# Performance work log

Hardware: AMD Instinct MI355X
Metric: run time of the kernel (lower is better)

## Reference

```python
import jax, jax.numpy as jnp
import numpy as np

B, N, C, G, K = 4, 6000, 91, 32, 100
IMG = 800.0
SCORE_TH = 0.05
NMS_TH = 0.5
MATCH_TH = 0.5
MIN_SIZE = 0.01
BBOX_CLIP = float(np.log(1000.0 / 16.0))
WX, WY, WW, WH = 10.0, 10.0, 5.0, 5.0


def _make_boxes(key, shape_prefix):
    k1, k2 = jax.random.split(key)
    xy = jax.random.uniform(k1, shape_prefix + (2,), minval=0.0, maxval=IMG - 130.0)
    wh = jax.random.uniform(k2, shape_prefix + (2,), minval=8.0, maxval=128.0)
    return jnp.concatenate([xy, xy + wh], axis=-1)


def setup_inputs() -> dict:
    key = jax.random.key(0)
    k1, k2, k3, k4, k5 = jax.random.split(key, 5)
    return {
        "class_logits": 2.0 * jax.random.normal(k1, (B * N, C), dtype=jnp.float32),
        "box_regression": jax.random.normal(k2, (B * N, C * 4), dtype=jnp.float32),
        "proposals": _make_boxes(k3, (B, N)),
        "gt_boxes": _make_boxes(k4, (B, G)),
        "gt_labels": jax.random.randint(k5, (B, G), 1, C),
    }


def _box_iou(a, b):
    # a [G,4], b [N,4] -> [G,N]
    area_a = (a[:, 2] - a[:, 0]) * (a[:, 3] - a[:, 1])
    area_b = (b[:, 2] - b[:, 0]) * (b[:, 3] - b[:, 1])
    lt = jnp.maximum(a[:, None, :2], b[None, :, :2])
    rb = jnp.minimum(a[:, None, 2:], b[None, :, 2:])
    wh = jnp.clip(rb - lt, 0.0)
    inter = wh[..., 0] * wh[..., 1]
    return inter / (area_a[:, None] + area_b[None, :] - inter)


def _decode(rel, props):
    # torchvision BoxCoder.decode; rel [N,C,4], props [N,4]
    w = props[:, 2] - props[:, 0]
    h = props[:, 3] - props[:, 1]
    cx = props[:, 0] + 0.5 * w
    cy = props[:, 1] + 0.5 * h
    dx = rel[..., 0] / WX
    dy = rel[..., 1] / WY
    dw = jnp.minimum(rel[..., 2] / WW, BBOX_CLIP)
    dh = jnp.minimum(rel[..., 3] / WH, BBOX_CLIP)
    pcx = dx * w[:, None] + cx[:, None]
    pcy = dy * h[:, None] + cy[:, None]
    pw = jnp.exp(dw) * w[:, None]
    ph = jnp.exp(dh) * h[:, None]
    return jnp.stack([pcx - 0.5 * pw, pcy - 0.5 * ph, pcx + 0.5 * pw, pcy + 0.5 * ph], axis=-1)


def _image(logits, reg, props, gtb, gtl):
    # --- assign_targets_to_proposals (Matcher, low=high=0.5, no low-quality matches) ---
    iou = _box_iou(gtb, props)                      # [G, N]
    best = iou.max(axis=0)
    mi = jnp.argmax(iou, axis=0)
    matched = jnp.where(best >= MATCH_TH, mi, -1)   # -1 == BELOW_LOW_THRESHOLD
    assigned = jnp.where(matched >= 0, gtl[jnp.clip(matched, 0)], 0)

    # --- postprocess_detections ---
    scores = jax.nn.softmax(logits, axis=-1)[:, 1:].reshape(-1)                       # [N*(C-1)]
    boxes = jnp.clip(_decode(reg.reshape(N, C, 4), props)[:, 1:], 0.0, IMG)
    boxes = boxes.reshape(-1, 4)                                                      # [N*(C-1),4]
    labels = jnp.tile(jnp.arange(1, C), N)                                            # [N*(C-1)]
    ws = boxes[:, 2] - boxes[:, 0]
    hs = boxes[:, 3] - boxes[:, 1]
    valid = (scores > SCORE_TH) & (ws >= MIN_SIZE) & (hs >= MIN_SIZE)
    s0 = jnp.where(valid, scores, -jnp.inf)
    # batched_nms trick: offset boxes by label so cross-class IoU is 0
    off = boxes + (labels.astype(boxes.dtype) * (IMG + 1.0))[:, None]
    off_area = (off[:, 2] - off[:, 0]) * (off[:, 3] - off[:, 1])

    def step(s, _):
        i = jnp.argmax(s)
        sc = s[i]
        b = off[i]
        lt = jnp.maximum(off[:, :2], b[:2])
        rb = jnp.minimum(off[:, 2:], b[2:])
        wh = jnp.clip(rb - lt, 0.0)
        inter = wh[:, 0] * wh[:, 1]
        iou_all = inter / (off_area + (b[2] - b[0]) * (b[3] - b[1]) - inter)
        s = jnp.where(iou_all > NMS_TH, -jnp.inf, s)  # suppress (includes self)
        ok = jnp.isfinite(sc)
        ob = jnp.where(ok, boxes[i], 0.0)
        osc = jnp.where(ok, sc, 0.0)
        ol = jnp.where(ok, labels[i], -1)
        return s, (ob, osc, ol)

    _, (kb, ksc, kl) = jax.lax.scan(step, s0, None, length=K)
    return kb, ksc, kl, assigned, matched


def reference(class_logits, box_regression, proposals, gt_boxes, gt_labels):
    logits = class_logits.reshape(B, N, C)
    reg = box_regression.reshape(B, N, C * 4)
    kb, ksc, kl, assigned, matched = jax.vmap(_image)(logits, reg, proposals, gt_boxes, gt_labels)
    dets = jnp.concatenate([kb, ksc[..., None]], axis=-1)  # [B, K, 5]
    return dets, kl, assigned, matched
```

## Files before the change

### kernel.cpp

```cpp
#include <hip/hip_runtime.h>
#include <math.h>

#define NB 4
#define NN 6000
#define NC 91
#define NG 32
#define NK 100
#define NCLS (NC - 1)
#define NBUC (NB * NCLS)
#define SLOTS_MAX 2048
#define CUR_STRIDE 32
#define PMAX 512
#define MATW 256
#define MPB 4096
#define RS_BLOCKS 6000

#define SCORE_TH 0.05f
#define NMS_TH 0.5f
#define MATCH_TH 0.5f
#define MIN_SIZE 0.01f
#define BBOX_CLIP 4.135166556742356f
#define C_SUP 0.5000000298023223876953125

#define CFENCE() asm volatile("" ::: "memory")

__device__ __forceinline__ bool decode_one(
    const float* __restrict__ reg, const float* __restrict__ props,
    float l, float m, float s0, int row, int c, float out[5])
{
    float score = __fdiv_rn(expf(__fsub_rn(l, m)), s0);

    const float4 p = *reinterpret_cast<const float4*>(props + (size_t)row * 4);
    float w  = __fsub_rn(p.z, p.x);
    float h  = __fsub_rn(p.w, p.y);
    float cx = __fadd_rn(p.x, __fmul_rn(0.5f, w));
    float cy = __fadd_rn(p.y, __fmul_rn(0.5f, h));

    const float4 r4 = *reinterpret_cast<const float4*>(
        reg + (size_t)row * (NC * 4) + (size_t)c * 4);
    float dx = __fdiv_rn(r4.x, 10.0f);
    float dy = __fdiv_rn(r4.y, 10.0f);
    float dw = fminf(__fdiv_rn(r4.z, 5.0f), BBOX_CLIP);
    float dh = fminf(__fdiv_rn(r4.w, 5.0f), BBOX_CLIP);

    float pcx = __fadd_rn(__fmul_rn(dx, w), cx);
    float pcy = __fadd_rn(__fmul_rn(dy, h), cy);
    float pw  = __fmul_rn(expf(dw), w);
    float ph  = __fmul_rn(expf(dh), h);

    float x1 = __fsub_rn(pcx, __fmul_rn(0.5f, pw));
    float y1 = __fsub_rn(pcy, __fmul_rn(0.5f, ph));
    float x2 = __fadd_rn(pcx, __fmul_rn(0.5f, pw));
    float y2 = __fadd_rn(pcy, __fmul_rn(0.5f, ph));
    x1 = fminf(fmaxf(x1, 0.0f), 800.0f);
    y1 = fminf(fmaxf(y1, 0.0f), 800.0f);
    x2 = fminf(fmaxf(x2, 0.0f), 800.0f);
    y2 = fminf(fmaxf(y2, 0.0f), 800.0f);

    out[0] = score; out[1] = x1; out[2] = y1; out[3] = x2; out[4] = y2;
    float ws_ = __fsub_rn(x2, x1);
    float hs_ = __fsub_rn(y2, y1);
    return (score > SCORE_TH) && (ws_ >= MIN_SIZE) && (hs_ >= MIN_SIZE);
}

__global__ __launch_bounds__(256) void fused_kernel(
    const float* __restrict__ logits, const float* __restrict__ reg,
    const float* __restrict__ props, const float* __restrict__ gtb,
    const int* __restrict__ gtl,
    float* __restrict__ out_assigned, float* __restrict__ out_matched,
    int* __restrict__ cursors, float* __restrict__ ent, int slots)
{
    int bid = blockIdx.x;
    if (bid < RS_BLOCKS) {
        int wid = threadIdx.x >> 6, lane = threadIdx.x & 63;
        int row = bid * 4 + wid;
        const float* rp = logits + (size_t)row * NC;
        float l0 = rp[lane];
        float l1 = (lane < NC - 64) ? rp[64 + lane] : -INFINITY;
        float m = fmaxf(fmaxf(-INFINITY, l0), l1);
        for (int o = 32; o; o >>= 1) m = fmaxf(m, __shfl_down(m, o));
        m = __shfl(m, 0);
        float s = __fadd_rn(__fadd_rn(0.0f, expf(__fsub_rn(l0, m))),
                            expf(__fsub_rn(l1, m)));
        for (int o = 32; o; o >>= 1) s = __fadd_rn(s, __shfl_down(s, o));
        float s0 = __shfl(s, 0);
        float thr = __fadd_rn(m, logf(__fmul_rn(0.04f, s0)));

        int b = row / NN;
        int nprop = row - b * NN;

        if (lane >= 1 && l0 > thr) {
            float o[5];
            if (decode_one(reg, props, l0, m, s0, row, lane, o)) {
                int c = lane;
                int g = b * NCLS + (c - 1);
                int pos = atomicAdd(&cursors[g * CUR_STRIDE], 1);
                if (pos < slots) {
                    float* e = ent + ((size_t)g * slots + pos) * 8;
                    *reinterpret_cast<float4*>(e) =
                        make_float4(o[1], o[2], o[3], o[4]);
                    *reinterpret_cast<float2*>(e + 4) =
                        make_float2(o[0], (float)(nprop * NCLS + (c - 1)));
                }
            }
        }
        if (lane < NC - 64 && l1 > thr) {
            float o[5];
            int c = lane + 64;
            if (decode_one(reg, props, l1, m, s0, row, c, o)) {
                int g = b * NCLS + (c - 1);
                int pos = atomicAdd(&cursors[g * CUR_STRIDE], 1);
                if (pos < slots) {
                    float* e = ent + ((size_t)g * slots + pos) * 8;
                    *reinterpret_cast<float4*>(e) =
                        make_float4(o[1], o[2], o[3], o[4]);
                    *reinterpret_cast<float2*>(e + 4) =
                        make_float2(o[0], (float)(nprop * NCLS + (c - 1)));
                }
            }
        }
    } else {
        int t = (bid - RS_BLOCKS) * 256 + threadIdx.x;
        if (t >= NB * NN) return;
        int b = t / NN;
        const float4 p = *reinterpret_cast<const float4*>(props + (size_t)t * 4);
        float parea = __fmul_rn(__fsub_rn(p.z, p.x), __fsub_rn(p.w, p.y));
        float best = -1.0f; int bi = -1;
        for (int g = 0; g < NG; ++g) {
            const float4 q = *reinterpret_cast<const float4*>(gtb + ((size_t)b * NG + g) * 4);
            float garea = __fmul_rn(__fsub_rn(q.z, q.x), __fsub_rn(q.w, q.y));
            float ltx = fmaxf(q.x, p.x), lty = fmaxf(q.y, p.y);
            float rbx = fminf(q.z, p.z), rby = fminf(q.w, p.w);
            float wx = fmaxf(__fsub_rn(rbx, ltx), 0.0f);
            float wy = fmaxf(__fsub_rn(rby, lty), 0.0f);
            float inter = __fmul_rn(wx, wy);
            float iou = __fdiv_rn(inter, __fsub_rn(__fadd_rn(garea, parea), inter));
            if (iou > best) { best = iou; bi = g; }
        }
        int matched = (best >= MATCH_TH) ? bi : -1;
        int assigned = (matched >= 0) ? gtl[b * NG + matched] : 0;
        out_matched[t]  = (float)matched;
        out_assigned[t] = (float)assigned;
    }
}

__device__ void nms_glb(int g, int n, float* __restrict__ E, float tb, float cls,
                        float* __restrict__ selbuf, int* __restrict__ selcnt)
{
    int lane = threadIdx.x & 63;
    int kout = 0;
    for (int k = 0; k < NK; ++k) {
        float bv = -INFINITY, boi = INFINITY; int bi = -1;
        for (int i = lane; i < n; i += 64) {
            float v = E[(size_t)i * 8 + 4], oi = E[(size_t)i * 8 + 5];
            if (v > bv || (v == bv && oi < boi)) { bv = v; boi = oi; bi = i; }
        }
        int wl = lane;
        for (int o = 1; o < 64; o <<= 1) {
            float v2 = __shfl_xor(bv, o); float o2 = __shfl_xor(boi, o);
            int l2 = __shfl_xor(wl, o);
            bool bt = (v2 > bv) || (v2 == bv && o2 < boi);
            bv = bt ? v2 : bv; boi = bt ? o2 : boi; wl = bt ? l2 : wl;
        }
        if (bv == -INFINITY) break;
        int wi = __shfl(bi, wl);
        float sx1 = E[(size_t)wi * 8 + 0], sy1 = E[(size_t)wi * 8 + 1];
        float sx2 = E[(size_t)wi * 8 + 2], sy2 = E[(size_t)wi * 8 + 3];
        if (lane == wl) {
            float* so = selbuf + ((size_t)g * NK + k) * 8;
            so[0] = bv; so[1] = sx1; so[2] = sy1; so[3] = sx2; so[4] = sy2;
            so[5] = cls; so[6] = boi; so[7] = 0.0f;
        }
        float bx1 = __fadd_rn(sx1, tb), by1 = __fadd_rn(sy1, tb);
        float bx2 = __fadd_rn(sx2, tb), by2 = __fadd_rn(sy2, tb);
        float sar = __fmul_rn(__fsub_rn(bx2, bx1), __fsub_rn(by2, by1));
        for (int i = lane; i < n; i += 64) {
            float v = E[(size_t)i * 8 + 4];
            if (v == -INFINITY) continue;
            float ox1 = __fadd_rn(E[(size_t)i * 8 + 0], tb);
            float oy1 = __fadd_rn(E[(size_t)i * 8 + 1], tb);
            float ox2 = __fadd_rn(E[(size_t)i * 8 + 2], tb);
            float oy2 = __fadd_rn(E[(size_t)i * 8 + 3], tb);
            float oar = __fmul_rn(__fsub_rn(ox2, ox1), __fsub_rn(oy2, oy1));
            float ltx = fmaxf(ox1, bx1), lty = fmaxf(oy1, by1);
            float rbx = fminf(ox2, bx2), rby = fminf(oy2, by2);
            float wx = fmaxf(__fsub_rn(rbx, ltx), 0.0f);
            float wy = fmaxf(__fsub_rn(rby, lty), 0.0f);
            float inter = __fmul_rn(wx, wy);
            float den = __fsub_rn(__fadd_rn(oar, sar), inter);
            if ((double)inter > C_SUP * (double)den) E[(size_t)i * 8 + 4] = -INFINITY;
        }
        kout = k + 1;
    }
    if (lane == 0) selcnt[g] = kout;
}

template <int CAP>
__device__ __forceinline__ float selN(const float a[CAP], int j) {
    float r = a[0];
#pragma unroll
    for (int i = 1; i < CAP; ++i) r = (j == i) ? a[i] : r;
    return r;
}
__device__ __forceinline__ float rdlane(float v, int l) {
    return __uint_as_float(
        (unsigned)__builtin_amdgcn_readlane((int)__float_as_uint(v), l));
}

template <int CAP>
__device__ __forceinline__ int sweep_reg(
    int lane, int n, float tb,
    const float* sx1, const float* sy1, const float* sx2, const float* sy2,
    int* acc)
{
    float ox1[CAP], oy1[CAP], ox2[CAP], oy2[CAP], oar[CAP];
    unsigned alive = 0;
#pragma unroll
    for (int j = 0; j < CAP; ++j) {
        int sidx = lane * CAP + j;
        if (sidx < n) {
            float a  = __fadd_rn(sx1[sidx], tb);
            float b_ = __fadd_rn(sy1[sidx], tb);
            float c_ = __fadd_rn(sx2[sidx], tb);
            float d_ = __fadd_rn(sy2[sidx], tb);
            ox1[j] = a; oy1[j] = b_; ox2[j] = c_; oy2[j] = d_;
            oar[j] = __fmul_rn(__fsub_rn(c_, a), __fsub_rn(d_, b_));
            alive |= 1u << j;
        } else {
            ox1[j] = 0.f; oy1[j] = 0.f; ox2[j] = 0.f; oy2[j] = 0.f; oar[j] = 0.f;
        }
    }
    int kout = 0;
    while (kout < NK) {
        unsigned long long bal = __ballot(alive != 0u);
        if (!bal) break;
        int fl = (int)__ffsll(bal) - 1;
        unsigned am = (unsigned)__builtin_amdgcn_readlane((int)alive, fl);
        int js = __ffs(am) - 1;
        float bx1 = rdlane(selN<CAP>(ox1, js), fl);
        float by1 = rdlane(selN<CAP>(oy1, js), fl);
        float bx2 = rdlane(selN<CAP>(ox2, js), fl);
        float by2 = rdlane(selN<CAP>(oy2, js), fl);
        float bar = rdlane(selN<CAP>(oar, js), fl);
        if (lane == 0) acc[kout] = fl * CAP + js;
        kout++;
        unsigned kill = 0;
#pragma unroll
        for (int j = 0; j < CAP; ++j) {
            float ltx = fmaxf(ox1[j], bx1), lty = fmaxf(oy1[j], by1);
            float rbx = fminf(ox2[j], bx2), rby = fminf(oy2[j], by2);
            float wx = fmaxf(__fsub_rn(rbx, ltx), 0.0f);
            float wy = fmaxf(__fsub_rn(rby, lty), 0.0f);
            float inter = __fmul_rn(wx, wy);
            float den = __fsub_rn(__fadd_rn(oar[j], bar), inter);
            if ((double)inter > C_SUP * (double)den) kill |= 1u << j;
        }
        alive &= ~kill;
    }
    return kout;
}

__global__ __launch_bounds__(256) void bucket_nms_kernel(
    const int* __restrict__ cursors, int slots,
    float* __restrict__ entries,
    float* __restrict__ selbuf, int* __restrict__ selcnt)
{
    int g = blockIdx.x;
    int n = cursors[g * CUR_STRIDE]; if (n > slots) n = slots;
    int tid = threadIdx.x;
    if (n == 0) { if (tid == 0) selcnt[g] = 0; return; }
    float* E = entries + (size_t)g * slots * 8;
    float cls = (float)(g % NCLS + 1);
    float tb = __fmul_rn(cls, 801.0f);

    if (n > PMAX) {
        if (tid < 64) nms_glb(g, n, E, tb, cls, selbuf, selcnt);
        return;
    }

    __shared__ unsigned skhi[PMAX], sklo[PMAX];
    __shared__ int sperm[PMAX];
    __shared__ float sx1[PMAX], sy1[PMAX], sx2[PMAX], sy2[PMAX];
    __shared__ unsigned long long dmask[MATW * 4];
    __shared__ int acc[NK];
    __shared__ int s_kout, s_fb;

    int P = 64; while (P < n) P <<= 1;

    for (int i = tid; i < P; i += 256) {
        if (i < n) {
            const float2 kv = *reinterpret_cast<const float2*>(E + (size_t)i * 8 + 4);
            skhi[i] = __float_as_uint(kv.x);
            sklo[i] = ~((unsigned)kv.y);
        } else { skhi[i] = 0u; sklo[i] = 0u; }
        sperm[i] = i;
    }
    __syncthreads();
    for (int k = 2; k <= P; k <<= 1) {
        for (int j = k >> 1; j > 0; j >>= 1) {
            bool cross = (j >= 128);
            if (cross) __syncthreads();
            for (int t = tid; t < (P >> 1); t += 256) {
                int i = ((t & ~(j - 1)) << 1) | (t & (j - 1));
                int l = i | j;
                unsigned ah = skhi[i], al = sklo[i], ch = skhi[l], cl_ = sklo[l];
                bool alt = (ah < ch) || (ah == ch && al < cl_);
                bool agt = (ah > ch) || (ah == ch && al > cl_);
                bool sw = ((i & k) == 0) ? alt : agt;
                if (sw) {
                    skhi[i] = ch; sklo[i] = cl_; skhi[l] = ah; sklo[l] = al;
                    int tp = sperm[i]; sperm[i] = sperm[l]; sperm[l] = tp;
                }
            }
            if (cross) __syncthreads();
            else CFENCE();
        }
    }
    __syncthreads();
    for (int i = tid; i < n; i += 256) {
        const float4 v = *reinterpret_cast<const float4*>(E + (size_t)sperm[i] * 8);
        sx1[i] = v.x; sy1[i] = v.y; sx2[i] = v.z; sy2[i] = v.w;
    }
    __syncthreads();

    int W = (n < MATW) ? n : MATW;
    int nchunk = (W + 63) >> 6;
    int wv = tid >> 6, lane = tid & 63;

    float jx1[4], jy1[4], jx2[4], jy2[4], jar[4];
#pragma unroll
    for (int c = 0; c < 4; ++c) {
        int j = c * 64 + lane;
        if (j < W) {
            float a  = __fadd_rn(sx1[j], tb);
            float b_ = __fadd_rn(sy1[j], tb);
            float c_ = __fadd_rn(sx2[j], tb);
            float d_ = __fadd_rn(sy2[j], tb);
            jx1[c] = a; jy1[c] = b_; jx2[c] = c_; jy2[c] = d_;
            jar[c] = __fmul_rn(__fsub_rn(c_, a), __fsub_rn(d_, b_));
        } else {
            jx1[c] = 0.f; jy1[c] = 0.f; jx2[c] = 0.f; jy2[c] = 0.f; jar[c] = 0.f;
        }
    }
    {
        int i0 = wv;
        float nx1 = 0.f, ny1 = 0.f, nx2 = 0.f, ny2 = 0.f;
        if (i0 < W) { nx1 = sx1[i0]; ny1 = sy1[i0]; nx2 = sx2[i0]; ny2 = sy2[i0]; }
        for (int i = i0; i < W; i += 4) {
            float rx1 = nx1, ry1 = ny1, rx2 = nx2, ry2 = ny2;
            int ni = i + 4;
            if (ni < W) { nx1 = sx1[ni]; ny1 = sy1[ni]; nx2 = sx2[ni]; ny2 = sy2[ni]; }
            float bx1 = __fadd_rn(rx1, tb), by1 = __fadd_rn(ry1, tb);
            float bx2 = __fadd_rn(rx2, tb), by2 = __fadd_rn(ry2, tb);
            float bar = __fmul_rn(__fsub_rn(bx2, bx1), __fsub_rn(by2, by1));
            int ic = i >> 6;
#pragma unroll
            for (int c = 0; c < 4; ++c) {
                if (c >= ic && c < nchunk) {
                    bool jv = (c * 64 + lane) < W;
                    float ltx = fmaxf(jx1[c], bx1), lty = fmaxf(jy1[c], by1);
                    float rbx = fminf(jx2[c], bx2), rby = fminf(jy2[c], by2);
                    float wx = fmaxf(__fsub_rn(rbx, ltx), 0.0f);
                    float wy = fmaxf(__fsub_rn(rby, lty), 0.0f);
                    float inter = __fmul_rn(wx, wy);
                    float den = __fsub_rn(__fadd_rn(jar[c], bar), inter);
                    bool sup = jv && ((double)inter > C_SUP * (double)den);
                    unsigned long long w64 = __ballot(sup);
                    if (lane == 0) dmask[i * 4 + c] = w64;
                }
            }
        }
    }
    __syncthreads();

    if (tid < 64) {
        unsigned long long alive = 0ull;
        if (lane < nchunk) {
            int rem = W - (lane << 6);
            alive = (rem >= 64) ? ~0ull : ((1ull << rem) - 1ull);
        }
        int kout = 0;
        while (kout < NK) {
            unsigned long long bal = __ballot(alive != 0ull);
            if (!bal) break;
            int fl = (int)__ffsll(bal) - 1;
            unsigned long long am = __shfl(alive, fl);
            int js = (int)__ffsll(am) - 1;
            int cand = (fl << 6) + js;
            if (lane == 0) acc[kout] = cand;
            kout++;
            if (lane < nchunk) alive &= ~dmask[cand * 4 + lane];
        }
        if (lane == 0) {
            s_kout = kout;
            s_fb = (kout < NK && n > W) ? 1 : 0;
        }
    }
    __syncthreads();

    if (s_fb) {
        if (tid < 64) {
            int kout = sweep_reg<8>(lane, n, tb, sx1, sy1, sx2, sy2, acc);
            if (lane == 0) s_kout = kout;
        }
        __syncthreads();
    }

    int kc = s_kout;
    if (tid == 0) selcnt[g] = kc;
    for (int k = tid; k < kc; k += 256) {
        int cand = acc[k];
        float* so = selbuf + ((size_t)g * NK + k) * 8;
        so[0] = __uint_as_float(skhi[cand]);
        so[1] = sx1[cand]; so[2] = sy1[cand];
        so[3] = sx2[cand]; so[4] = sy2[cand];
        so[5] = cls; so[6] = (float)(~sklo[cand]); so[7] = 0.0f;
    }
}

__global__ __launch_bounds__(512) void merge_kernel(
    const float* __restrict__ selbuf, const int* __restrict__ selcnt,
    float* __restrict__ out_dets, float* __restrict__ out_kl)
{
    int b = blockIdx.x, tid = threadIdx.x;
    __shared__ int scnt[NCLS], soff[NCLS + 1];
    __shared__ unsigned akhi[512], aklo[512];
    __shared__ unsigned bkhi[MPB], bklo[MPB], bpay[MPB];
    __shared__ int s_T, s_cntA;
    __shared__ unsigned s_LBhi, s_LBlo;

    if (tid < NCLS) scnt[tid] = selcnt[b * NCLS + tid];
    if (tid == 0) s_T = 0;
    __syncthreads();
    if (tid == 0) {
        int a = 0, ca = 0;
        for (int c = 0; c < NCLS; ++c) {
            soff[c] = a; a += scnt[c];
            ca += (scnt[c] < 4 ? scnt[c] : 4);
        }
        soff[NCLS] = a; s_cntA = ca;
    }
    __syncthreads();
    int tot = soff[NCLS];

    if (tot == 0) {
        for (int z = tid; z < NK * 5; z += 512) out_dets[(size_t)b * NK * 5 + z] = 0.0f;
        for (int z = tid; z < NK; z += 512)     out_kl[(size_t)b * NK + z] = -1.0f;
        return;
    }

    {
        unsigned kh = 0u, kl = 0u;
        if (tid < NCLS * 4) {
            int c = tid >> 2, i = tid & 3;
            if (i < scnt[c]) {
                const float* e = selbuf + ((size_t)(b * NCLS + c) * NK + i) * 8;
                kh = __float_as_uint(e[0]); kl = ~((unsigned)e[6]);
            }
        }
        akhi[tid] = kh; aklo[tid] = kl;
    }
    __syncthreads();
    for (int k = 2; k <= 512; k <<= 1) {
        for (int j = k >> 1; j > 0; j >>= 1) {
            bool cross = (j >= 128);
            if (cross) __syncthreads();
            if (tid < 256) {
                int t = tid;
                int i = ((t & ~(j - 1)) << 1) | (t & (j - 1));
                int l = i | j;
                unsigned ah = akhi[i], al = aklo[i], ch = akhi[l], cl_ = aklo[l];
                bool alt = (ah < ch) || (ah == ch && al < cl_);
                bool agt = (ah > ch) || (ah == ch && al > cl_);
                bool sw = ((i & k) == 0) ? alt : agt;
                if (sw) {
                    akhi[i] = ch; aklo[i] = cl_; akhi[l] = ah; aklo[l] = al;
                }
            }
            if (cross) __syncthreads();
            else CFENCE();
        }
    }
    __syncthreads();
    if (tid == 0) {
        if (s_cntA >= NK) { s_LBhi = akhi[NK - 1]; s_LBlo = aklo[NK - 1]; }
        else              { s_LBhi = 0u;           s_LBlo = 0u; }
    }
    __syncthreads();
    unsigned LBhi = s_LBhi, LBlo = s_LBlo;

    for (int flat = tid; flat < tot; flat += 512) {
        int lo = 0, hi = NCLS - 1;
        while (lo < hi) { int mid = (lo + hi + 1) >> 1;
                          if (soff[mid] <= flat) lo = mid; else hi = mid - 1; }
        int c = lo, i = flat - soff[c];
        const float* e = selbuf + ((size_t)(b * NCLS + c) * NK + i) * 8;
        unsigned kh = __float_as_uint(e[0]), kl = ~((unsigned)e[6]);
        bool ge = (kh > LBhi) || (kh == LBhi && kl >= LBlo);
        if (ge) {
            int pos = atomicAdd(&s_T, 1);
            if (pos < MPB) { bkhi[pos] = kh; bklo[pos] = kl;
                             bpay[pos] = (unsigned)((c << 7) | i); }
        }
    }
    __syncthreads();
    int T = s_T;

    if (T > MPB) {
        if (tid >= 64) return;
        int lane = tid;
        int g0 = b * NCLS + lane;
        int g1 = (lane < NCLS - 64) ? g0 + 64 : -1;
        int c0 = scnt[lane];
        int c1 = (g1 >= 0) ? scnt[lane + 64] : 0;
        int p0 = 0, p1 = 0;
        unsigned long long k0c = 0, k1c = 0;
        if (p0 < c0) { const float* h = selbuf + ((size_t)g0 * NK) * 8;
            k0c = ((unsigned long long)__float_as_uint(h[0]) << 32) | (unsigned long long)(~(unsigned)h[6]); }
        if (g1 >= 0 && p1 < c1) { const float* h = selbuf + ((size_t)g1 * NK) * 8;
            k1c = ((unsigned long long)__float_as_uint(h[0]) << 32) | (unsigned long long)(~(unsigned)h[6]); }
        for (int k = 0; k < NK; ++k) {
            bool t1 = (k1c > k0c);
            unsigned long long bk = t1 ? k1c : k0c;
            int bslot = t1 ? (lane + 64) : lane;
            for (int o = 1; o < 64; o <<= 1) {
                unsigned long long k2 = __shfl_xor(bk, o);
                int b2 = __shfl_xor(bslot, o);
                if (k2 > bk) { bk = k2; bslot = b2; }
            }
            if (bk == 0ull) {
                for (int z = k * 5 + lane; z < NK * 5; z += 64)
                    out_dets[(size_t)b * NK * 5 + z] = 0.0f;
                for (int z = k + lane; z < NK; z += 64)
                    out_kl[(size_t)b * NK + z] = -1.0f;
                return;
            }
            int owner = bslot & 63;
            if (lane == owner) {
                bool isA = (bslot < 64);
                int gg = isA ? g0 : g1;
                int pp = isA ? p0 : p1;
                const float* e = selbuf + ((size_t)gg * NK + pp) * 8;
                size_t o = ((size_t)b * NK + k) * 5;
                out_dets[o + 0] = e[1]; out_dets[o + 1] = e[2];
                out_dets[o + 2] = e[3]; out_dets[o + 3] = e[4];
                out_dets[o + 4] = e[0];
                out_kl[(size_t)b * NK + k] = e[5];
                if (isA) {
                    p0++; k0c = 0;
                    if (p0 < c0) { const float* h = selbuf + ((size_t)g0 * NK + p0) * 8;
                        k0c = ((unsigned long long)__float_as_uint(h[0]) << 32) | (unsigned long long)(~(unsigned)h[6]); }
                } else {
                    p1++; k1c = 0;
                    if (p1 < c1) { const float* h = selbuf + ((size_t)g1 * NK + p1) * 8;
                        k1c = ((unsigned long long)__float_as_uint(h[0]) << 32) | (unsigned long long)(~(unsigned)h[6]); }
                }
            }
        }
        return;
    }

    int P = 128; while (P < T) P <<= 1;
    for (int i = T + tid; i < P; i += 512) { bkhi[i] = 0u; bklo[i] = 0u; bpay[i] = 0u; }
    __syncthreads();
    for (int k = 2; k <= P; k <<= 1) {
        for (int j = k >> 1; j > 0; j >>= 1) {
            bool cross = (j >= 128);
            if (cross) __syncthreads();
            for (int t = tid; t < (P >> 1); t += 512) {
                int i = ((t & ~(j - 1)) << 1) | (t & (j - 1));
                int l = i | j;
                unsigned ah = bkhi[i], al = bklo[i], ch = bkhi[l], cl_ = bklo[l];
                bool alt = (ah < ch) || (ah == ch && al < cl_);
                bool agt = (ah > ch) || (ah == ch && al > cl_);
                bool sw = ((i & k) == 0) ? alt : agt;
                if (sw) {
                    bkhi[i] = ch; bklo[i] = cl_; bkhi[l] = ah; bklo[l] = al;
                    unsigned tp = bpay[i]; bpay[i] = bpay[l]; bpay[l] = tp;
                }
            }
            if (cross) __syncthreads();
            else CFENCE();
        }
    }
    __syncthreads();
    int kc = (T < NK) ? T : NK;
    for (int k = tid; k < NK; k += 512) {
        size_t o = ((size_t)b * NK + k) * 5;
        if (k < kc) {
            unsigned pay = bpay[k];
            int c = (int)(pay >> 7), p = (int)(pay & 127);
            const float* e = selbuf + ((size_t)(b * NCLS + c) * NK + p) * 8;
            out_dets[o + 0] = e[1]; out_dets[o + 1] = e[2];
            out_dets[o + 2] = e[3]; out_dets[o + 3] = e[4];
            out_dets[o + 4] = e[0];
            out_kl[(size_t)b * NK + k] = e[5];
        } else {
            out_dets[o + 0] = 0.0f; out_dets[o + 1] = 0.0f;
            out_dets[o + 2] = 0.0f; out_dets[o + 3] = 0.0f;
            out_dets[o + 4] = 0.0f;
            out_kl[(size_t)b * NK + k] = -1.0f;
        }
    }
}

extern "C" void kernel_launch(void* const* d_in, const int* in_sizes, int n_in,
                              void* d_out, int out_size, void* d_ws, size_t ws_size,
                              hipStream_t stream) {
    const float* logits = (const float*)d_in[0];
    const float* reg    = (const float*)d_in[1];
    const float* props  = (const float*)d_in[2];
    const float* gtb    = (const float*)d_in[3];
    const int*   gtl    = (const int*)d_in[4];

    float* out          = (float*)d_out;
    float* out_dets     = out;
    float* out_kl       = out + NB * NK * 5;
    float* out_assigned = out_kl + NB * NK;
    float* out_matched  = out_assigned + NB * NN;

    char* ws = (char*)d_ws;
    int*   cursors = (int*)(ws + 0);
    int*   selcnt  = (int*)(ws + 49152);
    float* selbuf  = (float*)(ws + 53248);
    size_t off_ent = 1205248;

    long avail = (long)ws_size - (long)off_ent;
    long per_slot = 32L * NBUC;
    long slotsl = (avail > 0) ? avail / per_slot : 0;
    int slots = (int)((slotsl > SLOTS_MAX) ? SLOTS_MAX : (slotsl < 0 ? 0 : slotsl));

    float* entries = (float*)(ws + off_ent);

    hipMemsetAsync(cursors, 0, NBUC * CUR_STRIDE * sizeof(int), stream);
    const int MATCH_BLOCKS = (NB * NN + 255) / 256;
    fused_kernel<<<RS_BLOCKS + MATCH_BLOCKS, 256, 0, stream>>>(
        logits, reg, props, gtb, gtl, out_assigned, out_matched,
        cursors, entries, slots);
    bucket_nms_kernel<<<NBUC, 256, 0, stream>>>(
        cursors, slots, entries, selbuf, selcnt);
    merge_kernel<<<NB, 512, 0, stream>>>(selbuf, selcnt, out_dets, out_kl);
}
```

Before: 122.9 us.

## Split bucket NMS into sort/matrix kernel and a separate 64-thread sweep kernel

The per-bucket NMS kernel is split in two. The first kernel sorts, builds the suppression bitmask matrix and writes the matrix and permutation to global memory. A new single-wave kernel then runs the greedy sweep and any fallback. PMAX is raised so that larger buckets stay off the slow global-memory path, and SLOTS_MAX is halved. The aim is to stop a 256-thread block from idling while one wave does the serial sweep, at the cost of an extra launch, global round-trips and a larger workspace footprint.

After: 132.0 us. 1.07x slower.

```diff
diff --git a/kernel.cpp b/kernel.cpp
--- a/kernel.cpp
+++ b/kernel.cpp
@@ -8,9 +8,9 @@
 #define NK 100
 #define NCLS (NC - 1)
 #define NBUC (NB * NCLS)
-#define SLOTS_MAX 2048
+#define SLOTS_MAX 1024
 #define CUR_STRIDE 32
-#define PMAX 512
+#define PMAX 1024
 #define MATW 256
 #define MPB 4096
 #define RS_BLOCKS 6000
@@ -260,30 +260,33 @@
     return kout;
 }
 
-__global__ __launch_bounds__(256) void bucket_nms_kernel(
+__global__ __launch_bounds__(256) void sort_matrix_kernel(
     const int* __restrict__ cursors, int slots,
     float* __restrict__ entries,
+    unsigned* __restrict__ permG, unsigned long long* __restrict__ dmaskG,
+    int2* __restrict__ binfo,
     float* __restrict__ selbuf, int* __restrict__ selcnt)
 {
     int g = blockIdx.x;
     int n = cursors[g * CUR_STRIDE]; if (n > slots) n = slots;
     int tid = threadIdx.x;
-    if (n == 0) { if (tid == 0) selcnt[g] = 0; return; }
+    if (n == 0) {
+        if (tid == 0) { selcnt[g] = 0; binfo[g] = make_int2(1, 0); }
+        return;
+    }
     float* E = entries + (size_t)g * slots * 8;
     float cls = (float)(g % NCLS + 1);
     float tb = __fmul_rn(cls, 801.0f);
 
     if (n > PMAX) {
         if (tid < 64) nms_glb(g, n, E, tb, cls, selbuf, selcnt);
+        if (tid == 0) binfo[g] = make_int2(1, n);
         return;
     }
 
     __shared__ unsigned skhi[PMAX], sklo[PMAX];
     __shared__ int sperm[PMAX];
     __shared__ float sx1[PMAX], sy1[PMAX], sx2[PMAX], sy2[PMAX];
-    __shared__ unsigned long long dmask[MATW * 4];
-    __shared__ int acc[NK];
-    __shared__ int s_kout, s_fb;
 
     int P = 64; while (P < n) P <<= 1;
 
@@ -366,55 +369,79 @@
                     float den = __fsub_rn(__fadd_rn(jar[c], bar), inter);
                     bool sup = jv && ((double)inter > C_SUP * (double)den);
                     unsigned long long w64 = __ballot(sup);
-                    if (lane == 0) dmask[i * 4 + c] = w64;
+                    if (lane == 0) dmaskG[(size_t)g * PMAX + i * 4 + c] = w64;
                 }
             }
         }
     }
-    __syncthreads();
-
-    if (tid < 64) {
-        unsigned long long alive = 0ull;
-        if (lane < nchunk) {
-            int rem = W - (lane << 6);
-            alive = (rem >= 64) ? ~0ull : ((1ull << rem) - 1ull);
-        }
-        int kout = 0;
-        while (kout < NK) {
-            unsigned long long bal = __ballot(alive != 0ull);
-            if (!bal) break;
-            int fl = (int)__ffsll(bal) - 1;
-            unsigned long long am = __shfl(alive, fl);
-            int js = (int)__ffsll(am) - 1;
-            int cand = (fl << 6) + js;
-            if (lane == 0) acc[kout] = cand;
-            kout++;
-            if (lane < nchunk) alive &= ~dmask[cand * 4 + lane];
-        }
-        if (lane == 0) {
-            s_kout = kout;
-            s_fb = (kout < NK && n > W) ? 1 : 0;
-        }
-    }
-    __syncthreads();
-
-    if (s_fb) {
-        if (tid < 64) {
-            int kout = sweep_reg<8>(lane, n, tb, sx1, sy1, sx2, sy2, acc);
-            if (lane == 0) s_kout = kout;
+    for (int i = tid; i < n; i += 256) permG[(size_t)g * PMAX + i] = (unsigned)sperm[i];
+    if (tid == 0) binfo[g] = make_int2(0, n);
+}
+
+__global__ __launch_bounds__(64) void sweep_kernel(
+    int slots, const float* __restrict__ entries,
+    const unsigned* __restrict__ permG,
+    const unsigned long long* __restrict__ dmaskG,
+    const int2* __restrict__ binfo,
+    float* __restrict__ selbuf, int* __restrict__ selcnt)
+{
+    int g = blockIdx.x;
+    int lane = threadIdx.x;
+    int2 bi = binfo[g];
+    if (bi.x) return;
+    int n = bi.y;
+    const float* E = entries + (size_t)g * slots * 8;
+    float cls = (float)(g % NCLS + 1);
+    float tb = __fmul_rn(cls, 801.0f);
+
+    int W = (n < MATW) ? n : MATW;
+    int nchunk = (W + 63) >> 6;
+
+    __shared__ unsigned long long dm[MATW * 4];
+    __shared__ int acc[NK];
+    __shared__ float fx1[PMAX], fy1[PMAX], fx2[PMAX], fy2[PMAX];
+
+    for (int t = lane; t < W * 4; t += 64) dm[t] = dmaskG[(size_t)g * PMAX + t];
+    __syncthreads();
+
+    unsigned long long alive = 0ull;
+    if (lane < nchunk) {
+        int rem = W - (lane << 6);
+        alive = (rem >= 64) ? ~0ull : ((1ull << rem) - 1ull);
+    }
+    int kout = 0;
+    while (kout < NK) {
+        unsigned long long bal = __ballot(alive != 0ull);
+        if (!bal) break;
+        int fl = (int)__ffsll(bal) - 1;
+        unsigned long long am = __shfl(alive, fl);
+        int js = (int)__ffsll(am) - 1;
+        int cand = (fl << 6) + js;
+        if (lane == 0) acc[kout] = cand;
+        kout++;
+        if (lane < nchunk) alive &= ~dm[cand * 4 + lane];
+    }
+
+    if (kout < NK && n > W) {
+        for (int i = lane; i < n; i += 64) {
+            unsigned sl = permG[(size_t)g * PMAX + i];
+            const float4 v = *reinterpret_cast<const float4*>(E + (size_t)sl * 8);
+            fx1[i] = v.x; fy1[i] = v.y; fx2[i] = v.z; fy2[i] = v.w;
         }
         __syncthreads();
-    }
-
-    int kc = s_kout;
-    if (tid == 0) selcnt[g] = kc;
-    for (int k = tid; k < kc; k += 256) {
+        kout = sweep_reg<16>(lane, n, tb, fx1, fy1, fx2, fy2, acc);
+    }
+    __syncthreads();
+    if (lane == 0) selcnt[g] = kout;
+
+    for (int k = lane; k < kout; k += 64) {
         int cand = acc[k];
+        unsigned sl = permG[(size_t)g * PMAX + cand];
+        const float* e = E + (size_t)sl * 8;
         float* so = selbuf + ((size_t)g * NK + k) * 8;
-        so[0] = __uint_as_float(skhi[cand]);
-        so[1] = sx1[cand]; so[2] = sy1[cand];
-        so[3] = sx2[cand]; so[4] = sy2[cand];
-        so[5] = cls; so[6] = (float)(~sklo[cand]); so[7] = 0.0f;
+        so[0] = e[4];
+        so[1] = e[0]; so[2] = e[1]; so[3] = e[2]; so[4] = e[3];
+        so[5] = cls; so[6] = e[5]; so[7] = 0.0f;
     }
 }
 
@@ -622,8 +649,12 @@
     char* ws = (char*)d_ws;
     int*   cursors = (int*)(ws + 0);
     int*   selcnt  = (int*)(ws + 49152);
-    float* selbuf  = (float*)(ws + 53248);
-    size_t off_ent = 1205248;
+    int2*  binfo   = (int2*)(ws + 51200);
+    float* selbuf  = (float*)(ws + 57344);
+    unsigned* permG = (unsigned*)(ws + 1212416);
+    unsigned long long* dmaskG =
+        (unsigned long long*)(ws + 2686976);
+    size_t off_ent = 5636096;
 
     long avail = (long)ws_size - (long)off_ent;
     long per_slot = 32L * NBUC;
@@ -637,7 +668,9 @@
     fused_kernel<<<RS_BLOCKS + MATCH_BLOCKS, 256, 0, stream>>>(
         logits, reg, props, gtb, gtl, out_assigned, out_matched,
         cursors, entries, slots);
-    bucket_nms_kernel<<<NBUC, 256, 0, stream>>>(
-        cursors, slots, entries, selbuf, selcnt);
+    sort_matrix_kernel<<<NBUC, 256, 0, stream>>>(
+        cursors, slots, entries, permG, dmaskG, binfo, selbuf, selcnt);
+    sweep_kernel<<<NBUC, 64, 0, stream>>>(
+        slots, entries, permG, dmaskG, binfo, selbuf, selcnt);
     merge_kernel<<<NB, 512, 0, stream>>>(selbuf, selcnt, out_dets, out_kl);
 }
```

## Replace bitonic sort with rank sort and drop global-memory NMS fallback

Applied to the files above, without the earlier changes.

Replaces the in-shared-memory bitonic sort of per-bucket candidates with a counting (rank) sort in which each thread computes the rank of up to four elements by scanning all keys. PMAX is raised to 1024 and SLOTS_MAX lowered to 1024, so every bucket takes the shared-memory path and the slow single-wavefront global NMS fallback is removed. The register sweep capacity is doubled to cover the larger buckets. The trade-off is O(n^2) comparisons per bucket, more shared memory per block, and candidates beyond 1024 per bucket being dropped if they ever occur.

Result: slower. 142.4 us (+15.8%).

```diff
diff --git a/kernel.cpp b/kernel.cpp
--- a/kernel.cpp
+++ b/kernel.cpp
@@ -8,9 +8,9 @@
 #define NK 100
 #define NCLS (NC - 1)
 #define NBUC (NB * NCLS)
-#define SLOTS_MAX 2048
+#define SLOTS_MAX 1024
 #define CUR_STRIDE 32
-#define PMAX 512
+#define PMAX 1024
 #define MATW 256
 #define MPB 4096
 #define RS_BLOCKS 6000
@@ -142,57 +142,6 @@
         out_matched[t]  = (float)matched;
         out_assigned[t] = (float)assigned;
     }
-}
-
-__device__ void nms_glb(int g, int n, float* __restrict__ E, float tb, float cls,
-                        float* __restrict__ selbuf, int* __restrict__ selcnt)
-{
-    int lane = threadIdx.x & 63;
-    int kout = 0;
-    for (int k = 0; k < NK; ++k) {
-        float bv = -INFINITY, boi = INFINITY; int bi = -1;
-        for (int i = lane; i < n; i += 64) {
-            float v = E[(size_t)i * 8 + 4], oi = E[(size_t)i * 8 + 5];
-            if (v > bv || (v == bv && oi < boi)) { bv = v; boi = oi; bi = i; }
-        }
-        int wl = lane;
-        for (int o = 1; o < 64; o <<= 1) {
-            float v2 = __shfl_xor(bv, o); float o2 = __shfl_xor(boi, o);
-            int l2 = __shfl_xor(wl, o);
-            bool bt = (v2 > bv) || (v2 == bv && o2 < boi);
-            bv = bt ? v2 : bv; boi = bt ? o2 : boi; wl = bt ? l2 : wl;
-        }
-        if (bv == -INFINITY) break;
-        int wi = __shfl(bi, wl);
-        float sx1 = E[(size_t)wi * 8 + 0], sy1 = E[(size_t)wi * 8 + 1];
-        float sx2 = E[(size_t)wi * 8 + 2], sy2 = E[(size_t)wi * 8 + 3];
-        if (lane == wl) {
-            float* so = selbuf + ((size_t)g * NK + k) * 8;
-            so[0] = bv; so[1] = sx1; so[2] = sy1; so[3] = sx2; so[4] = sy2;
-            so[5] = cls; so[6] = boi; so[7] = 0.0f;
-        }
-        float bx1 = __fadd_rn(sx1, tb), by1 = __fadd_rn(sy1, tb);
-        float bx2 = __fadd_rn(sx2, tb), by2 = __fadd_rn(sy2, tb);
-        float sar = __fmul_rn(__fsub_rn(bx2, bx1), __fsub_rn(by2, by1));
-        for (int i = lane; i < n; i += 64) {
-            float v = E[(size_t)i * 8 + 4];
-            if (v == -INFINITY) continue;
-            float ox1 = __fadd_rn(E[(size_t)i * 8 + 0], tb);
-            float oy1 = __fadd_rn(E[(size_t)i * 8 + 1], tb);
-            float ox2 = __fadd_rn(E[(size_t)i * 8 + 2], tb);
-            float oy2 = __fadd_rn(E[(size_t)i * 8 + 3], tb);
-            float oar = __fmul_rn(__fsub_rn(ox2, ox1), __fsub_rn(oy2, oy1));
-            float ltx = fmaxf(ox1, bx1), lty = fmaxf(oy1, by1);
-            float rbx = fminf(ox2, bx2), rby = fminf(oy2, by2);
-            float wx = fmaxf(__fsub_rn(rbx, ltx), 0.0f);
-            float wy = fmaxf(__fsub_rn(rby, lty), 0.0f);
-            float inter = __fmul_rn(wx, wy);
-            float den = __fsub_rn(__fadd_rn(oar, sar), inter);
-            if ((double)inter > C_SUP * (double)den) E[(size_t)i * 8 + 4] = -INFINITY;
-        }
-        kout = k + 1;
-    }
-    if (lane == 0) selcnt[g] = kout;
 }
 
 template <int CAP>
@@ -273,50 +222,43 @@
     float cls = (float)(g % NCLS + 1);
     float tb = __fmul_rn(cls, 801.0f);
 
-    if (n > PMAX) {
-        if (tid < 64) nms_glb(g, n, E, tb, cls, selbuf, selcnt);
-        return;
-    }
-
-    __shared__ unsigned skhi[PMAX], sklo[PMAX];
+    __shared__ unsigned khi[PMAX], klo[PMAX];
     __shared__ int sperm[PMAX];
     __shared__ float sx1[PMAX], sy1[PMAX], sx2[PMAX], sy2[PMAX];
     __shared__ unsigned long long dmask[MATW * 4];
     __shared__ int acc[NK];
     __shared__ int s_kout, s_fb;
 
-    int P = 64; while (P < n) P <<= 1;
-
-    for (int i = tid; i < P; i += 256) {
-        if (i < n) {
-            const float2 kv = *reinterpret_cast<const float2*>(E + (size_t)i * 8 + 4);
-            skhi[i] = __float_as_uint(kv.x);
-            sklo[i] = ~((unsigned)kv.y);
-        } else { skhi[i] = 0u; sklo[i] = 0u; }
-        sperm[i] = i;
-    }
-    __syncthreads();
-    for (int k = 2; k <= P; k <<= 1) {
-        for (int j = k >> 1; j > 0; j >>= 1) {
-            bool cross = (j >= 128);
-            if (cross) __syncthreads();
-            for (int t = tid; t < (P >> 1); t += 256) {
-                int i = ((t & ~(j - 1)) << 1) | (t & (j - 1));
-                int l = i | j;
-                unsigned ah = skhi[i], al = sklo[i], ch = skhi[l], cl_ = sklo[l];
-                bool alt = (ah < ch) || (ah == ch && al < cl_);
-                bool agt = (ah > ch) || (ah == ch && al > cl_);
-                bool sw = ((i & k) == 0) ? alt : agt;
-                if (sw) {
-                    skhi[i] = ch; sklo[i] = cl_; skhi[l] = ah; sklo[l] = al;
-                    int tp = sperm[i]; sperm[i] = sperm[l]; sperm[l] = tp;
-                }
-            }
-            if (cross) __syncthreads();
-            else CFENCE();
-        }
-    }
-    __syncthreads();
+    for (int i = tid; i < n; i += 256) {
+        const float2 kv = *reinterpret_cast<const float2*>(E + (size_t)i * 8 + 4);
+        khi[i] = __float_as_uint(kv.x);
+        klo[i] = ~((unsigned)kv.y);
+    }
+    __syncthreads();
+
+    {
+        int e0 = tid, e1 = tid + 256, e2 = tid + 512, e3 = tid + 768;
+        bool v0 = e0 < n, v1 = e1 < n, v2 = e2 < n, v3 = e3 < n;
+        unsigned h0 = 0, l0 = 0, h1 = 0, l1 = 0, h2 = 0, l2 = 0, h3 = 0, l3 = 0;
+        if (v0) { h0 = khi[e0]; l0 = klo[e0]; }
+        if (v1) { h1 = khi[e1]; l1 = klo[e1]; }
+        if (v2) { h2 = khi[e2]; l2 = klo[e2]; }
+        if (v3) { h3 = khi[e3]; l3 = klo[e3]; }
+        int r0 = 0, r1 = 0, r2 = 0, r3 = 0;
+        for (int j = 0; j < n; ++j) {
+            unsigned hj = khi[j], lj = klo[j];
+            r0 += (int)((hj > h0) | ((hj == h0) & (lj > l0)));
+            r1 += (int)((hj > h1) | ((hj == h1) & (lj > l1)));
+            r2 += (int)((hj > h2) | ((hj == h2) & (lj > l2)));
+            r3 += (int)((hj > h3) | ((hj == h3) & (lj > l3)));
+        }
+        if (v0) sperm[r0] = e0;
+        if (v1) sperm[r1] = e1;
+        if (v2) sperm[r2] = e2;
+        if (v3) sperm[r3] = e3;
+    }
+    __syncthreads();
+
     for (int i = tid; i < n; i += 256) {
         const float4 v = *reinterpret_cast<const float4*>(E + (size_t)sperm[i] * 8);
         sx1[i] = v.x; sy1[i] = v.y; sx2[i] = v.z; sy2[i] = v.w;
@@ -400,7 +342,7 @@
 
     if (s_fb) {
         if (tid < 64) {
-            int kout = sweep_reg<8>(lane, n, tb, sx1, sy1, sx2, sy2, acc);
+            int kout = sweep_reg<16>(lane, n, tb, sx1, sy1, sx2, sy2, acc);
             if (lane == 0) s_kout = kout;
         }
         __syncthreads();
@@ -410,11 +352,11 @@
     if (tid == 0) selcnt[g] = kc;
     for (int k = tid; k < kc; k += 256) {
         int cand = acc[k];
+        const float* e = E + (size_t)sperm[cand] * 8;
         float* so = selbuf + ((size_t)g * NK + k) * 8;
-        so[0] = __uint_as_float(skhi[cand]);
-        so[1] = sx1[cand]; so[2] = sy1[cand];
-        so[3] = sx2[cand]; so[4] = sy2[cand];
-        so[5] = cls; so[6] = (float)(~sklo[cand]); so[7] = 0.0f;
+        so[0] = e[4];
+        so[1] = e[0]; so[2] = e[1]; so[3] = e[2]; so[4] = e[3];
+        so[5] = cls; so[6] = e[5]; so[7] = 0.0f;
     }
 }
 
```
